# Optimization experiments

Measured on AMD Instinct MI355X. Metric: run time of the kernel, lower is better.

## Reference

```python
import jax, jax.numpy as jnp
import numpy as np

T, N, F_IN, H1, H2, F_OUT = 48, 4096, 64, 64, 32, 64

def setup_inputs() -> dict:
    key = jax.random.key(0)
    ks = jax.random.split(key, 14)
    sc = 0.05
    x = jax.random.normal(ks[0], (T, N, F_IN), jnp.float32)
    adj = jax.random.uniform(ks[1], (N, N), jnp.float32) / N  # roughly row-normalized dense adjacency
    fc_w = jax.random.normal(ks[2], (F_IN, H1), jnp.float32) * sc
    fc_b = jnp.zeros((H1,), jnp.float32)
    Wz = jax.random.normal(ks[3], (H1, F_OUT), jnp.float32) * sc
    Wr = jax.random.normal(ks[4], (H1, F_OUT), jnp.float32) * sc
    Wh = jax.random.normal(ks[5], (H1, F_OUT), jnp.float32) * sc
    Lz = jax.random.normal(ks[6], (2 * F_OUT, F_OUT), jnp.float32) * sc
    Lr = jax.random.normal(ks[7], (2 * F_OUT, F_OUT), jnp.float32) * sc
    Lh = jax.random.normal(ks[8], (2 * F_OUT, F_OUT), jnp.float32) * sc
    bz = jnp.zeros((F_OUT,), jnp.float32)
    br = jnp.zeros((F_OUT,), jnp.float32)
    bh = jnp.zeros((F_OUT,), jnp.float32)
    return {"x": x, "adj": adj, "fc_w": fc_w, "fc_b": fc_b,
            "Wz": Wz, "Wr": Wr, "Wh": Wh,
            "Lz": Lz, "Lr": Lr, "Lh": Lh,
            "bz": bz, "br": br, "bh": bh}

def reference(x, adj, fc_w, fc_b, Wz, Wr, Wh, Lz, Lr, Lh, bz, br, bh):
    # relu(fc(x)) followed by relu(unsqueeze) == single relu
    xh = jax.nn.relu(x @ fc_w + fc_b)          # [T, N, H1]
    h0 = jnp.zeros((N, F_OUT), x.dtype)

    def step(h, xi):
        # TGCN cell: dense graph conv A @ (X W) feeding GRU-style gates
        az = adj @ (xi @ Wz)                   # [N, F_OUT]
        ar = adj @ (xi @ Wr)
        ah = adj @ (xi @ Wh)
        z = jax.nn.sigmoid(jnp.concatenate([az, h], axis=-1) @ Lz + bz)
        r = jax.nn.sigmoid(jnp.concatenate([ar, h], axis=-1) @ Lr + br)
        h_tilde = jnp.tanh(jnp.concatenate([ah, h * r], axis=-1) @ Lh + bh)
        h_new = z * h + (1.0 - z) * h_tilde
        return h_new, None

    h, _ = jax.lax.scan(step, h0, xh)
    return h[None]                              # [1, N, F_OUT]
```

## Files before the change

kernel.cpp:

```cpp
#include <hip/hip_runtime.h>

typedef unsigned short u16;
typedef unsigned char u8;
typedef short s16x8 __attribute__((ext_vector_type(8)));
typedef unsigned short u16x4 __attribute__((ext_vector_type(4)));
typedef float f32x4 __attribute__((ext_vector_type(4)));
typedef int i32x4 __attribute__((ext_vector_type(4)));
typedef int i32x8 __attribute__((ext_vector_type(8)));

#define AS1 __attribute__((address_space(1)))
#define AS3 __attribute__((address_space(3)))

__device__ __forceinline__ void g2l16(const void* g, void* l) {
  __builtin_amdgcn_global_load_lds((const AS1 void*)g, (AS3 void*)l, 16, 0, 0);
}

__device__ __forceinline__ float b2f(u16 u) {
  union { unsigned int i; float f; } x; x.i = ((unsigned int)u) << 16; return x.f;
}
__device__ __forceinline__ u16 f2b(float f) {
  unsigned int u = __builtin_bit_cast(unsigned int, f);
  return (u16)((u + 0x7fffu + ((u >> 16) & 1u)) >> 16);
}
__device__ __forceinline__ u8 f2e4m3(float v) {
  int p = __builtin_amdgcn_cvt_pk_fp8_f32(v, 0.f, 0, false);
  return (u8)(p & 0xff);
}
__device__ __forceinline__ float sigm(float x) { return 1.f / (1.f + __expf(-x)); }
__device__ __forceinline__ float tanh_f(float x) { return 2.f / (1.f + __expf(-2.f * x)) - 1.f; }


__global__ __launch_bounds__(256) void kprep(
    const float* __restrict__ a, u8* __restrict__ ab,
    const float* __restrict__ fcw,
    const float* __restrict__ Wz, const float* __restrict__ Wr, const float* __restrict__ Wh,
    const float* __restrict__ Lz, const float* __restrict__ Lr, const float* __restrict__ Lh,
    u16* __restrict__ fcwT, u16* __restrict__ wct, u16* __restrict__ lbt) {
  int b = blockIdx.x, t = threadIdx.x;
  if (b < 4096) {
    size_t idx = (size_t)b * 256 + t;
    const float4* src = (const float4*)a;
    unsigned int* dst = (unsigned int*)ab;
#pragma unroll
    for (int k = 0; k < 4; ++k) {
      float4 v = src[idx + (size_t)k * 1048576];
      unsigned int p = __builtin_amdgcn_cvt_pk_fp8_f32(v.x * 4096.f, v.y * 4096.f, 0, false);
      p = __builtin_amdgcn_cvt_pk_fp8_f32(v.z * 4096.f, v.w * 4096.f, p, true);
      dst[idx + (size_t)k * 1048576] = p;
    }
    return;
  }
  int bb = b - 4096;
  if (bb < 48) {
    int idx = bb * 256 + t;
    int c_cat = idx >> 6, hh = idx & 63;
    int g = c_cat >> 6, c = c_cat & 63;
    const float* W = (g == 0) ? Wz : (g == 1) ? Wr : Wh;
    const float* L = (g == 0) ? Lz : (g == 1) ? Lr : Lh;
    float acc = 0.f;
    for (int m = 0; m < 64; ++m) acc += W[hh * 64 + m] * L[m * 64 + c];
    wct[c_cat * 64 + hh] = f2b(acc);
  } else if (bb == 48) {
    for (int i = 0; i < 16; ++i) {
      int idx = t * 16 + i; int hh = idx >> 6, f = idx & 63;
      fcwT[hh * 64 + f] = f2b(fcw[f * 64 + hh]);
    }
  } else {
    int g = bb - 49;
    const float* L = (g == 0) ? Lz : (g == 1) ? Lr : Lh;
    for (int i = 0; i < 16; ++i) {
      int idx = t * 16 + i; int c = idx >> 6, hh = idx & 63;
      lbt[g * 4096 + c * 64 + hh] = f2b(L[(64 + hh) * 64 + c]);
    }
  }
}

__global__ __launch_bounds__(256) void k1(
    const float* __restrict__ x, const float* __restrict__ fcb,
    const u16* __restrict__ fcwT, u8* __restrict__ xht) {
  __shared__ __align__(16) u16 xs[128 * 72];
  __shared__ __align__(16) u16 fw[64 * 72];
  __shared__ __align__(16) u8 xh8[64 * 128];
  __shared__ float fb[64];
  int tid = threadIdx.x, w = tid >> 6, l = tid & 63;
  int t = blockIdx.y, n0 = blockIdx.x * 128;
#pragma unroll
  for (int i2 = 0; i2 < 2; ++i2) {
    int g = tid + 256 * i2;
    s16x8 v = *(const s16x8*)&fcwT[g * 8];
    *(s16x8*)&fw[(g >> 3) * 72 + (g & 7) * 8] = v;
  }
  const float4* xg = (const float4*)(x + ((size_t)t * 4096 + n0) * 64);
#pragma unroll
  for (int i = 0; i < 8; ++i) {
    int f = tid + i * 256;
    float4 v = xg[f];
    u16x4 p; p[0] = f2b(v.x); p[1] = f2b(v.y); p[2] = f2b(v.z); p[3] = f2b(v.w);
    *(u16x4*)&xs[(f >> 4) * 72 + (f & 15) * 4] = p;
  }
  if (tid < 64) fb[tid] = fcb[tid];
  __syncthreads();

  int lm = l & 15, q = l >> 4;
  f32x4 acc[4][2];
#pragma unroll
  for (int i = 0; i < 4; ++i)
#pragma unroll
    for (int j = 0; j < 2; ++j)
#pragma unroll
      for (int r = 0; r < 4; ++r) acc[i][j][r] = 0.f;
#pragma unroll
  for (int s = 0; s < 2; ++s) {
    s16x8 af[4], bf[2];
#pragma unroll
    for (int i = 0; i < 4; ++i) af[i] = *(const s16x8*)&fw[(16 * i + lm) * 72 + 32 * s + q * 8];
#pragma unroll
    for (int j = 0; j < 2; ++j) bf[j] = *(const s16x8*)&xs[(32 * w + 16 * j + lm) * 72 + 32 * s + q * 8];
#pragma unroll
    for (int i = 0; i < 4; ++i)
#pragma unroll
      for (int j = 0; j < 2; ++j)
        acc[i][j] = __builtin_amdgcn_mfma_f32_16x16x32_bf16(af[i], bf[j], acc[i][j], 0, 0, 0);
  }
#pragma unroll
  for (int i = 0; i < 4; ++i)
#pragma unroll
    for (int j = 0; j < 2; ++j) {
      int node = 32 * w + 16 * j + lm;
      int h0 = 16 * i + q * 4;
#pragma unroll
      for (int r = 0; r < 4; ++r) {
        float v = acc[i][j][r] + fb[h0 + r];
        xh8[(h0 + r) * 128 + node] = f2e4m3(v > 0.f ? v : 0.f);
      }
    }
  __syncthreads();
  {
    int h = tid >> 2, seg = tid & 3;
    u8* dst = xht + (size_t)(t * 64 + h) * 4096 + n0 + seg * 32;
    const u8* src = &xh8[h * 128 + seg * 32];
    *(i32x4*)dst = *(const i32x4*)src;
    *(i32x4*)(dst + 16) = *(const i32x4*)(src + 16);
  }
}

__global__ __launch_bounds__(256) void k2(
    const u8* __restrict__ A, const u8* __restrict__ B, u16* __restrict__ M) {
  __shared__ __align__(16) u8 sh[32768];
  u8* As = sh;
  u8* Bs = sh + 16384;
  int tid = threadIdx.x, w = tid >> 6, l = tid & 63;
  int nt = blockIdx.x, mt = blockIdx.y;
  const u8* Ab = A + (size_t)mt * 128 * 4096;
  const u8* Bb = B + (size_t)nt * 128 * 4096;
  int lm = l & 15, q = l >> 4;
  int wm = w >> 1, wn = w & 1;
  f32x4 acc[4][4];
#pragma unroll
  for (int i = 0; i < 4; ++i)
#pragma unroll
    for (int j = 0; j < 4; ++j)
#pragma unroll
      for (int r = 0; r < 4; ++r) acc[i][j][r] = 0.f;
  for (int k0b = 0; k0b < 4096; k0b += 128) {
#pragma unroll
    for (int j = 0; j < 4; ++j) {
      int r0 = 32 * w + 8 * j;
      int row = r0 + (l >> 3);
      int c = ((l & 7) - row) & 7;
      size_t go = (size_t)row * 4096 + k0b + c * 16;
      g2l16(Ab + go, (char*)As + r0 * 128);
      g2l16(Bb + go, (char*)Bs + r0 * 128);
    }
    __syncthreads();
    i32x8 a8[4], b8[4];
#pragma unroll
    for (int i = 0; i < 4; ++i) {
      int ra = 64 * wm + 16 * i + lm;
      int p0 = (2 * q + ra) & 7, p1 = (2 * q + 1 + ra) & 7;
      i32x4 lo = *(const i32x4*)&As[ra * 128 + p0 * 16];
      i32x4 hi = *(const i32x4*)&As[ra * 128 + p1 * 16];
      a8[i] = __builtin_shufflevector(lo, hi, 0, 1, 2, 3, 4, 5, 6, 7);
      int rb = 64 * wn + 16 * i + lm;
      int q0 = (2 * q + rb) & 7, q1 = (2 * q + 1 + rb) & 7;
      i32x4 lo2 = *(const i32x4*)&Bs[rb * 128 + q0 * 16];
      i32x4 hi2 = *(const i32x4*)&Bs[rb * 128 + q1 * 16];
      b8[i] = __builtin_shufflevector(lo2, hi2, 0, 1, 2, 3, 4, 5, 6, 7);
    }
#pragma unroll
    for (int i = 0; i < 4; ++i)
#pragma unroll
      for (int j = 0; j < 4; ++j)
        acc[i][j] = __builtin_amdgcn_mfma_scale_f32_16x16x128_f8f6f4(
            a8[i], b8[j], acc[i][j], 0, 0, 0, 127, 0, 127);
    __syncthreads();
  }
  u16* tb = (u16*)sh;
  const float sc = 1.f / 4096.f;
#pragma unroll
  for (int p = 0; p < 2; ++p) {
    if (p) __syncthreads();
    if (wm == p) {
#pragma unroll
      for (int i = 0; i < 4; ++i)
#pragma unroll
        for (int j = 0; j < 4; ++j)
#pragma unroll
          for (int r = 0; r < 4; ++r)
            tb[(16 * i + 4 * q + r) * 136 + 64 * wn + 16 * j + lm] = f2b(acc[i][j][r] * sc);
    }
    __syncthreads();
    int row = tid >> 2, seg = tid & 3;
    u16* dst = M + (size_t)(mt * 128 + p * 64 + row) * 3072 + nt * 128 + seg * 32;
    const u16* src = &tb[row * 136 + seg * 32];
    *(i32x4*)dst = *(const i32x4*)src;
    *(i32x4*)(dst + 8)  = *(const i32x4*)(src + 8);
    *(i32x4*)(dst + 16) = *(const i32x4*)(src + 16);
    *(i32x4*)(dst + 24) = *(const i32x4*)(src + 24);
  }
}

__global__ __launch_bounds__(256) void k3(
    const u16* __restrict__ M, const u16* __restrict__ wct, const u16* __restrict__ lbt,
    const float* __restrict__ bz, const float* __restrict__ br, const float* __restrict__ bh,
    float* __restrict__ out) {
  __shared__ __align__(16) u16 hhi[16 * 72], hlo[16 * 72];
  __shared__ __align__(16) u16 rhi[16 * 72], rlo[16 * 72];
  int tid = threadIdx.x, w = tid >> 6, l = tid & 63;
  int nb0 = blockIdx.x * 16;
  int lm = l & 15, q = l >> 4;
  int cb = 16 * w + q * 4;
  s16x8 afw[3][2], afl[3][2];
#pragma unroll
  for (int g = 0; g < 3; ++g)
#pragma unroll
    for (int s = 0; s < 2; ++s) {
      afw[g][s] = *(const s16x8*)&wct[(size_t)(g * 64 + 16 * w + lm) * 64 + 32 * s + q * 8];
      afl[g][s] = *(const s16x8*)&lbt[(size_t)(g * 64 + 16 * w + lm) * 64 + 32 * s + q * 8];
    }
  for (int i = tid; i < 16 * 72; i += 256) { hhi[i] = 0; hlo[i] = 0; }
  f32x4 bzv, brv, bhv, hv;
#pragma unroll
  for (int r = 0; r < 4; ++r) {
    bzv[r] = bz[cb + r]; brv[r] = br[cb + r]; bhv[r] = bh[cb + r]; hv[r] = 0.f;
  }
  __syncthreads();

  const u16* Mrow = M + (size_t)(nb0 + lm) * 3072;
  s16x8 Mn[2];
  Mn[0] = *(const s16x8*)&Mrow[q * 8];
  Mn[1] = *(const s16x8*)&Mrow[32 + q * 8];

  for (int t = 0; t < 48; ++t) {
    s16x8 Mc[2] = {Mn[0], Mn[1]};
    if (t < 47) {
      Mn[0] = *(const s16x8*)&Mrow[(t + 1) * 64 + q * 8];
      Mn[1] = *(const s16x8*)&Mrow[(t + 1) * 64 + 32 + q * 8];
    }
    f32x4 uz, ur;
#pragma unroll
    for (int r = 0; r < 4; ++r) { uz[r] = 0.f; ur[r] = 0.f; }
#pragma unroll
    for (int s = 0; s < 2; ++s) {
      s16x8 hh = *(const s16x8*)&hhi[lm * 72 + 32 * s + q * 8];
      s16x8 hl = *(const s16x8*)&hlo[lm * 72 + 32 * s + q * 8];
      uz = __builtin_amdgcn_mfma_f32_16x16x32_bf16(afw[0][s], Mc[s], uz, 0, 0, 0);
      uz = __builtin_amdgcn_mfma_f32_16x16x32_bf16(afl[0][s], hh, uz, 0, 0, 0);
      uz = __builtin_amdgcn_mfma_f32_16x16x32_bf16(afl[0][s], hl, uz, 0, 0, 0);
      ur = __builtin_amdgcn_mfma_f32_16x16x32_bf16(afw[1][s], Mc[s], ur, 0, 0, 0);
      ur = __builtin_amdgcn_mfma_f32_16x16x32_bf16(afl[1][s], hh, ur, 0, 0, 0);
      ur = __builtin_amdgcn_mfma_f32_16x16x32_bf16(afl[1][s], hl, ur, 0, 0, 0);
    }
    f32x4 zv, rv;
#pragma unroll
    for (int r = 0; r < 4; ++r) {
      zv[r] = sigm(uz[r] + bzv[r]);
      rv[r] = sigm(ur[r] + brv[r]);
    }
    {
      u16x4 phi, plo;
#pragma unroll
      for (int r = 0; r < 4; ++r) {
        float p = hv[r] * rv[r];
        u16 hi = f2b(p); phi[r] = hi; plo[r] = f2b(p - b2f(hi));
      }
      *(u16x4*)&rhi[lm * 72 + cb] = phi;
      *(u16x4*)&rlo[lm * 72 + cb] = plo;
    }
    __syncthreads();
    f32x4 uh;
#pragma unroll
    for (int r = 0; r < 4; ++r) uh[r] = 0.f;
#pragma unroll
    for (int s = 0; s < 2; ++s) {
      s16x8 rh = *(const s16x8*)&rhi[lm * 72 + 32 * s + q * 8];
      s16x8 rl = *(const s16x8*)&rlo[lm * 72 + 32 * s + q * 8];
      uh = __builtin_amdgcn_mfma_f32_16x16x32_bf16(afw[2][s], Mc[s], uh, 0, 0, 0);
      uh = __builtin_amdgcn_mfma_f32_16x16x32_bf16(afl[2][s], rh, uh, 0, 0, 0);
      uh = __builtin_amdgcn_mfma_f32_16x16x32_bf16(afl[2][s], rl, uh, 0, 0, 0);
    }
    {
      u16x4 phi, plo;
#pragma unroll
      for (int r = 0; r < 4; ++r) {
        float th = tanh_f(uh[r] + bhv[r]);
        float hn = zv[r] * hv[r] + (1.f - zv[r]) * th;
        hv[r] = hn;
        u16 hi = f2b(hn); phi[r] = hi; plo[r] = f2b(hn - b2f(hi));
      }
      *(u16x4*)&hhi[lm * 72 + cb] = phi;
      *(u16x4*)&hlo[lm * 72 + cb] = plo;
    }
    __syncthreads();
  }
#pragma unroll
  for (int r = 0; r < 4; ++r)
    out[(size_t)(nb0 + lm) * 64 + cb + r] = hv[r];
}

extern "C" void kernel_launch(void* const* d_in, const int* in_sizes, int n_in,
                              void* d_out, int out_size, void* d_ws, size_t ws_size,
                              hipStream_t stream) {
  const float* x   = (const float*)d_in[0];
  const float* adj = (const float*)d_in[1];
  const float* fcw = (const float*)d_in[2];
  const float* fcb = (const float*)d_in[3];
  const float* Wz  = (const float*)d_in[4];
  const float* Wr  = (const float*)d_in[5];
  const float* Wh  = (const float*)d_in[6];
  const float* Lz  = (const float*)d_in[7];
  const float* Lr  = (const float*)d_in[8];
  const float* Lh  = (const float*)d_in[9];
  const float* bz  = (const float*)d_in[10];
  const float* br  = (const float*)d_in[11];
  const float* bh  = (const float*)d_in[12];
  char* ws = (char*)d_ws;
  u8*  xht  = (u8*)(ws);
  u8*  adj8 = (u8*)(ws + (size_t)12582912);
  u16* Mm   = (u16*)(ws + (size_t)29360128);
  u16* fcwT = (u16*)(ws + (size_t)54525952);
  u16* wct  = (u16*)(ws + (size_t)54534144);
  u16* lbt  = (u16*)(ws + (size_t)54558720);
  float* outp = (float*)d_out;

  hipLaunchKernelGGL(kprep, dim3(4148), dim3(256), 0, stream,
                     adj, adj8, fcw, Wz, Wr, Wh, Lz, Lr, Lh, fcwT, wct, lbt);
  hipLaunchKernelGGL(k1, dim3(32, 48), dim3(256), 0, stream, x, fcb, fcwT, xht);
  hipLaunchKernelGGL(k2, dim3(24, 32), dim3(256), 0, stream, adj8, xht, Mm);
  hipLaunchKernelGGL(k3, dim3(256), dim3(256), 0, stream, Mm, wct, lbt, bz, br, bh, outp);
}
```

Before: 282.9 us.

## Merge prep and fc kernels, widen GEMM N-tile, split gate accumulators

```diff
diff --git a/kernel.cpp b/kernel.cpp
--- a/kernel.cpp
+++ b/kernel.cpp
@@ -30,15 +30,16 @@
 __device__ __forceinline__ float tanh_f(float x) { return 2.f / (1.f + __expf(-2.f * x)) - 1.f; }
 
 
-__global__ __launch_bounds__(256) void kprep(
+__global__ __launch_bounds__(256) void kpre(
     const float* __restrict__ a, u8* __restrict__ ab,
-    const float* __restrict__ fcw,
+    const float* __restrict__ fcw, const float* __restrict__ fcb,
+    const float* __restrict__ x, u8* __restrict__ xht,
     const float* __restrict__ Wz, const float* __restrict__ Wr, const float* __restrict__ Wh,
     const float* __restrict__ Lz, const float* __restrict__ Lr, const float* __restrict__ Lh,
-    u16* __restrict__ fcwT, u16* __restrict__ wct, u16* __restrict__ lbt) {
-  int b = blockIdx.x, t = threadIdx.x;
+    u16* __restrict__ wct, u16* __restrict__ lbt) {
+  int b = blockIdx.x, tid = threadIdx.x;
   if (b < 4096) {
-    size_t idx = (size_t)b * 256 + t;
+    size_t idx = (size_t)b * 256 + tid;
     const float4* src = (const float4*)a;
     unsigned int* dst = (unsigned int*)ab;
 #pragma unroll
@@ -50,9 +51,8 @@
     }
     return;
   }
-  int bb = b - 4096;
-  if (bb < 48) {
-    int idx = bb * 256 + t;
+  if (b < 4144) {
+    int idx = (b - 4096) * 256 + tid;
     int c_cat = idx >> 6, hh = idx & 63;
     int g = c_cat >> 6, c = c_cat & 63;
     const float* W = (g == 0) ? Wz : (g == 1) ? Wr : Wh;
@@ -60,35 +60,29 @@
     float acc = 0.f;
     for (int m = 0; m < 64; ++m) acc += W[hh * 64 + m] * L[m * 64 + c];
     wct[c_cat * 64 + hh] = f2b(acc);
-  } else if (bb == 48) {
-    for (int i = 0; i < 16; ++i) {
-      int idx = t * 16 + i; int hh = idx >> 6, f = idx & 63;
-      fcwT[hh * 64 + f] = f2b(fcw[f * 64 + hh]);
-    }
-  } else {
-    int g = bb - 49;
+    return;
+  }
+  if (b < 4147) {
+    int g = b - 4144;
     const float* L = (g == 0) ? Lz : (g == 1) ? Lr : Lh;
     for (int i = 0; i < 16; ++i) {
-      int idx = t * 16 + i; int c = idx >> 6, hh = idx & 63;
+      int idx = tid * 16 + i; int c = idx >> 6, hh = idx & 63;
       lbt[g * 4096 + c * 64 + hh] = f2b(L[(64 + hh) * 64 + c]);
     }
-  }
-}
-
-__global__ __launch_bounds__(256) void k1(
-    const float* __restrict__ x, const float* __restrict__ fcb,
-    const u16* __restrict__ fcwT, u8* __restrict__ xht) {
+    return;
+  }
+  int kb = b - 4147;
+  int t = kb >> 5, n0 = (kb & 31) * 128;
   __shared__ __align__(16) u16 xs[128 * 72];
   __shared__ __align__(16) u16 fw[64 * 72];
   __shared__ __align__(16) u8 xh8[64 * 128];
   __shared__ float fb[64];
-  int tid = threadIdx.x, w = tid >> 6, l = tid & 63;
-  int t = blockIdx.y, n0 = blockIdx.x * 128;
-#pragma unroll
-  for (int i2 = 0; i2 < 2; ++i2) {
-    int g = tid + 256 * i2;
-    s16x8 v = *(const s16x8*)&fcwT[g * 8];
-    *(s16x8*)&fw[(g >> 3) * 72 + (g & 7) * 8] = v;
+  int w = tid >> 6, l = tid & 63;
+#pragma unroll
+  for (int i = 0; i < 16; ++i) {
+    int idx = tid + i * 256;
+    int h = idx & 63, f = idx >> 6;
+    fw[h * 72 + f] = f2b(fcw[f * 64 + h]);
   }
   const float4* xg = (const float4*)(x + ((size_t)t * 4096 + n0) * 64);
 #pragma unroll
@@ -146,34 +140,40 @@
 
 __global__ __launch_bounds__(256) void k2(
     const u8* __restrict__ A, const u8* __restrict__ B, u16* __restrict__ M) {
-  __shared__ __align__(16) u8 sh[32768];
+  __shared__ __align__(16) u8 sh[40960];
   u8* As = sh;
   u8* Bs = sh + 16384;
   int tid = threadIdx.x, w = tid >> 6, l = tid & 63;
   int nt = blockIdx.x, mt = blockIdx.y;
   const u8* Ab = A + (size_t)mt * 128 * 4096;
-  const u8* Bb = B + (size_t)nt * 128 * 4096;
+  const u8* Bb = B + (size_t)nt * 192 * 4096;
   int lm = l & 15, q = l >> 4;
   int wm = w >> 1, wn = w & 1;
-  f32x4 acc[4][4];
+  f32x4 acc[4][6];
 #pragma unroll
   for (int i = 0; i < 4; ++i)
 #pragma unroll
-    for (int j = 0; j < 4; ++j)
+    for (int j = 0; j < 6; ++j)
 #pragma unroll
       for (int r = 0; r < 4; ++r) acc[i][j][r] = 0.f;
+  int srow = l >> 3;
   for (int k0b = 0; k0b < 4096; k0b += 128) {
 #pragma unroll
     for (int j = 0; j < 4; ++j) {
       int r0 = 32 * w + 8 * j;
-      int row = r0 + (l >> 3);
+      int row = r0 + srow;
       int c = ((l & 7) - row) & 7;
-      size_t go = (size_t)row * 4096 + k0b + c * 16;
-      g2l16(Ab + go, (char*)As + r0 * 128);
-      g2l16(Bb + go, (char*)Bs + r0 * 128);
-    }
-    __syncthreads();
-    i32x8 a8[4], b8[4];
+      g2l16(Ab + (size_t)row * 4096 + k0b + c * 16, (char*)As + r0 * 128);
+    }
+#pragma unroll
+    for (int j = 0; j < 6; ++j) {
+      int r0 = 48 * w + 8 * j;
+      int row = r0 + srow;
+      int c = ((l & 7) - row) & 7;
+      g2l16(Bb + (size_t)row * 4096 + k0b + c * 16, (char*)Bs + r0 * 128);
+    }
+    __syncthreads();
+    i32x8 a8[4];
 #pragma unroll
     for (int i = 0; i < 4; ++i) {
       int ra = 64 * wm + 16 * i + lm;
@@ -181,18 +181,19 @@
       i32x4 lo = *(const i32x4*)&As[ra * 128 + p0 * 16];
       i32x4 hi = *(const i32x4*)&As[ra * 128 + p1 * 16];
       a8[i] = __builtin_shufflevector(lo, hi, 0, 1, 2, 3, 4, 5, 6, 7);
-      int rb = 64 * wn + 16 * i + lm;
+    }
+#pragma unroll
+    for (int j = 0; j < 6; ++j) {
+      int rb = 96 * wn + 16 * j + lm;
       int q0 = (2 * q + rb) & 7, q1 = (2 * q + 1 + rb) & 7;
       i32x4 lo2 = *(const i32x4*)&Bs[rb * 128 + q0 * 16];
       i32x4 hi2 = *(const i32x4*)&Bs[rb * 128 + q1 * 16];
-      b8[i] = __builtin_shufflevector(lo2, hi2, 0, 1, 2, 3, 4, 5, 6, 7);
-    }
-#pragma unroll
-    for (int i = 0; i < 4; ++i)
-#pragma unroll
-      for (int j = 0; j < 4; ++j)
+      i32x8 b8 = __builtin_shufflevector(lo2, hi2, 0, 1, 2, 3, 4, 5, 6, 7);
+#pragma unroll
+      for (int i = 0; i < 4; ++i)
         acc[i][j] = __builtin_amdgcn_mfma_scale_f32_16x16x128_f8f6f4(
-            a8[i], b8[j], acc[i][j], 0, 0, 0, 127, 0, 127);
+            a8[i], b8, acc[i][j], 0, 0, 0, 127, 0, 127);
+    }
     __syncthreads();
   }
   u16* tb = (u16*)sh;
@@ -204,19 +205,18 @@
 #pragma unroll
       for (int i = 0; i < 4; ++i)
 #pragma unroll
-        for (int j = 0; j < 4; ++j)
+        for (int j = 0; j < 6; ++j)
 #pragma unroll
           for (int r = 0; r < 4; ++r)
-            tb[(16 * i + 4 * q + r) * 136 + 64 * wn + 16 * j + lm] = f2b(acc[i][j][r] * sc);
+            tb[(16 * i + 4 * q + r) * 200 + 96 * wn + 16 * j + lm] = f2b(acc[i][j][r] * sc);
     }
     __syncthreads();
     int row = tid >> 2, seg = tid & 3;
-    u16* dst = M + (size_t)(mt * 128 + p * 64 + row) * 3072 + nt * 128 + seg * 32;
-    const u16* src = &tb[row * 136 + seg * 32];
-    *(i32x4*)dst = *(const i32x4*)src;
-    *(i32x4*)(dst + 8)  = *(const i32x4*)(src + 8);
-    *(i32x4*)(dst + 16) = *(const i32x4*)(src + 16);
-    *(i32x4*)(dst + 24) = *(const i32x4*)(src + 24);
+    u16* dst = M + (size_t)(mt * 128 + p * 64 + row) * 3072 + nt * 192 + seg * 48;
+    const u16* src = &tb[row * 200 + seg * 48];
+#pragma unroll
+    for (int v = 0; v < 6; ++v)
+      *(i32x4*)(dst + 8 * v) = *(const i32x4*)(src + 8 * v);
   }
 }
 
@@ -257,25 +257,25 @@
       Mn[0] = *(const s16x8*)&Mrow[(t + 1) * 64 + q * 8];
       Mn[1] = *(const s16x8*)&Mrow[(t + 1) * 64 + 32 + q * 8];
     }
-    f32x4 uz, ur;
-#pragma unroll
-    for (int r = 0; r < 4; ++r) { uz[r] = 0.f; ur[r] = 0.f; }
+    f32x4 uzw, uzh, urw, urh;
+#pragma unroll
+    for (int r = 0; r < 4; ++r) { uzw[r] = 0.f; uzh[r] = 0.f; urw[r] = 0.f; urh[r] = 0.f; }
 #pragma unroll
     for (int s = 0; s < 2; ++s) {
       s16x8 hh = *(const s16x8*)&hhi[lm * 72 + 32 * s + q * 8];
       s16x8 hl = *(const s16x8*)&hlo[lm * 72 + 32 * s + q * 8];
-      uz = __builtin_amdgcn_mfma_f32_16x16x32_bf16(afw[0][s], Mc[s], uz, 0, 0, 0);
-      uz = __builtin_amdgcn_mfma_f32_16x16x32_bf16(afl[0][s], hh, uz, 0, 0, 0);
-      uz = __builtin_amdgcn_mfma_f32_16x16x32_bf16(afl[0][s], hl, uz, 0, 0, 0);
-      ur = __builtin_amdgcn_mfma_f32_16x16x32_bf16(afw[1][s], Mc[s], ur, 0, 0, 0);
-      ur = __builtin_amdgcn_mfma_f32_16x16x32_bf16(afl[1][s], hh, ur, 0, 0, 0);
-      ur = __builtin_amdgcn_mfma_f32_16x16x32_bf16(afl[1][s], hl, ur, 0, 0, 0);
+      uzw = __builtin_amdgcn_mfma_f32_16x16x32_bf16(afw[0][s], Mc[s], uzw, 0, 0, 0);
+      uzh = __builtin_amdgcn_mfma_f32_16x16x32_bf16(afl[0][s], hh, uzh, 0, 0, 0);
+      uzh = __builtin_amdgcn_mfma_f32_16x16x32_bf16(afl[0][s], hl, uzh, 0, 0, 0);
+      urw = __builtin_amdgcn_mfma_f32_16x16x32_bf16(afw[1][s], Mc[s], urw, 0, 0, 0);
+      urh = __builtin_amdgcn_mfma_f32_16x16x32_bf16(afl[1][s], hh, urh, 0, 0, 0);
+      urh = __builtin_amdgcn_mfma_f32_16x16x32_bf16(afl[1][s], hl, urh, 0, 0, 0);
     }
     f32x4 zv, rv;
 #pragma unroll
     for (int r = 0; r < 4; ++r) {
-      zv[r] = sigm(uz[r] + bzv[r]);
-      rv[r] = sigm(ur[r] + brv[r]);
+      zv[r] = sigm(uzw[r] + uzh[r] + bzv[r]);
+      rv[r] = sigm(urw[r] + urh[r] + brv[r]);
     }
     {
       u16x4 phi, plo;
@@ -288,22 +288,22 @@
       *(u16x4*)&rlo[lm * 72 + cb] = plo;
     }
     __syncthreads();
-    f32x4 uh;
-#pragma unroll
-    for (int r = 0; r < 4; ++r) uh[r] = 0.f;
+    f32x4 uhw, uhh;
+#pragma unroll
+    for (int r = 0; r < 4; ++r) { uhw[r] = 0.f; uhh[r] = 0.f; }
 #pragma unroll
     for (int s = 0; s < 2; ++s) {
       s16x8 rh = *(const s16x8*)&rhi[lm * 72 + 32 * s + q * 8];
       s16x8 rl = *(const s16x8*)&rlo[lm * 72 + 32 * s + q * 8];
-      uh = __builtin_amdgcn_mfma_f32_16x16x32_bf16(afw[2][s], Mc[s], uh, 0, 0, 0);
-      uh = __builtin_amdgcn_mfma_f32_16x16x32_bf16(afl[2][s], rh, uh, 0, 0, 0);
-      uh = __builtin_amdgcn_mfma_f32_16x16x32_bf16(afl[2][s], rl, uh, 0, 0, 0);
+      uhw = __builtin_amdgcn_mfma_f32_16x16x32_bf16(afw[2][s], Mc[s], uhw, 0, 0, 0);
+      uhh = __builtin_amdgcn_mfma_f32_16x16x32_bf16(afl[2][s], rh, uhh, 0, 0, 0);
+      uhh = __builtin_amdgcn_mfma_f32_16x16x32_bf16(afl[2][s], rl, uhh, 0, 0, 0);
     }
     {
       u16x4 phi, plo;
 #pragma unroll
       for (int r = 0; r < 4; ++r) {
-        float th = tanh_f(uh[r] + bhv[r]);
+        float th = tanh_f(uhw[r] + uhh[r] + bhv[r]);
         float hn = zv[r] * hv[r] + (1.f - zv[r]) * th;
         hv[r] = hn;
         u16 hi = f2b(hn); phi[r] = hi; plo[r] = f2b(hn - b2f(hi));
@@ -338,14 +338,12 @@
   u8*  xht  = (u8*)(ws);
   u8*  adj8 = (u8*)(ws + (size_t)12582912);
   u16* Mm   = (u16*)(ws + (size_t)29360128);
-  u16* fcwT = (u16*)(ws + (size_t)54525952);
-  u16* wct  = (u16*)(ws + (size_t)54534144);
-  u16* lbt  = (u16*)(ws + (size_t)54558720);
+  u16* wct  = (u16*)(ws + (size_t)54525952);
+  u16* lbt  = (u16*)(ws + (size_t)54550528);
   float* outp = (float*)d_out;
 
-  hipLaunchKernelGGL(kprep, dim3(4148), dim3(256), 0, stream,
-                     adj, adj8, fcw, Wz, Wr, Wh, Lz, Lr, Lh, fcwT, wct, lbt);
-  hipLaunchKernelGGL(k1, dim3(32, 48), dim3(256), 0, stream, x, fcb, fcwT, xht);
-  hipLaunchKernelGGL(k2, dim3(24, 32), dim3(256), 0, stream, adj8, xht, Mm);
+  hipLaunchKernelGGL(kpre, dim3(5683), dim3(256), 0, stream,
+                     adj, adj8, fcw, fcb, x, xht, Wz, Wr, Wh, Lz, Lr, Lh, wct, lbt);
+  hipLaunchKernelGGL(k2, dim3(16, 32), dim3(256), 0, stream, adj8, xht, Mm);
   hipLaunchKernelGGL(k3, dim3(256), dim3(256), 0, stream, Mm, wct, lbt, bz, br, bh, outp);
 }
```

After: 261.1 us. 1.08x faster.
